# Optimization experiments

Measured on AMD Instinct MI355X. Metric: run time of the kernel, lower is better.

## Reference

```python
import jax, jax.numpy as jnp
import numpy as np

TOP_K = 6
N_GROUP = 8
TOPK_GROUP = 3
ROUTED_SCALING = 16.0
NORM_TOPK_PROB = False


def setup_inputs() -> dict:
    key = jax.random.key(0)
    k1, k2 = jax.random.split(key)
    hidden_states = jax.random.normal(k1, (4, 4096, 5120), dtype=jnp.float32)
    weight = jax.random.normal(k2, (160, 5120), dtype=jnp.float32) * 0.02
    return {"hidden_states": hidden_states, "weight": weight}


def _gate(hidden_states, weight):
    B, S, H = hidden_states.shape
    E = weight.shape[0]
    x = hidden_states.reshape(-1, H).astype(jnp.float32)  # [T, H]
    logits = jnp.einsum('th,eh->te', x, weight.astype(jnp.float32))  # [T, E]
    scores = jax.nn.softmax(logits, axis=-1)
    # group_limited_greedy: restrict experts to the topk_group best groups
    G = N_GROUP
    group_scores = scores.reshape(-1, G, E // G).max(axis=-1)  # [T, G]
    _, group_idx = jax.lax.top_k(group_scores, TOPK_GROUP)  # [T, topk_group]
    group_mask = jax.nn.one_hot(group_idx, G, dtype=jnp.bool_).any(axis=1)  # [T, G]
    score_mask = jnp.repeat(group_mask, E // G, axis=-1)  # [T, E]
    tmp_scores = jnp.where(score_mask, scores, 0.0)
    topk_weight, topk_idx = jax.lax.top_k(tmp_scores, TOP_K)
    if TOP_K > 1 and NORM_TOPK_PROB:
        topk_weight = topk_weight / (topk_weight.sum(axis=-1, keepdims=True) + 1e-20)
    else:
        topk_weight = topk_weight * ROUTED_SCALING
    return topk_idx, topk_weight


def reference(hidden_states, weight):
    return _gate(hidden_states, weight)
```

## Files before the change

kernel.cpp:

```cpp
#include <hip/hip_runtime.h>
#include <math.h>


#define TT    16384
#define HH    5120
#define EE    160
#define BT    32
#define BK    32
#define NT    (HH / BK)
#define SXLD  36
#define SWLD  161
#define SLF   161
#define TOPK  6

__device__ __forceinline__ bool betterf(float va, int ia, float vb, int ib) {
    return (va > vb) || ((va == vb) && (ia < ib));
}

__global__ __launch_bounds__(256)
void gate_kernel(const float* __restrict__ X, const float* __restrict__ W,
                 float* __restrict__ out) {
    __shared__ __align__(16) unsigned char smem_raw[2*BK*SXLD*4 + 2*BK*SWLD*4];
    float* sx    = (float*)smem_raw;
    float* sw    = sx + 2 * BK * SXLD;
    float* slogf = (float*)smem_raw;

    const int tid = threadIdx.x;
    const int tx  = tid & 31;
    const int ty  = tid >> 5;
    const long tok0 = (long)blockIdx.x * BT;

    double acc[4][5];
    #pragma unroll
    for (int j = 0; j < 4; ++j)
        #pragma unroll
        for (int m = 0; m < 5; ++m) acc[j][m] = 0.0;

    float4 px, pw[5];

    {
        int i = tid, tl = i >> 3, k4 = (i & 7) << 2;
        px = *(const float4*)(X + (tok0 + tl) * HH + k4);
        #pragma unroll
        for (int r = 0; r < 5; ++r) {
            int q = tid + 256 * r, e = q >> 3, kk = (q & 7) << 2;
            pw[r] = *(const float4*)(W + (long)e * HH + kk);
        }
        sx[(k4 + 0) * SXLD + tl] = px.x;
        sx[(k4 + 1) * SXLD + tl] = px.y;
        sx[(k4 + 2) * SXLD + tl] = px.z;
        sx[(k4 + 3) * SXLD + tl] = px.w;
        #pragma unroll
        for (int r = 0; r < 5; ++r) {
            int q = tid + 256 * r, e = q >> 3, kk = (q & 7) << 2;
            sw[(kk + 0) * SWLD + e] = pw[r].x;
            sw[(kk + 1) * SWLD + e] = pw[r].y;
            sw[(kk + 2) * SWLD + e] = pw[r].z;
            sw[(kk + 3) * SWLD + e] = pw[r].w;
        }
    }
    __syncthreads();

    for (int t = 0; t < NT; ++t) {
        const int cur = t & 1;
        if (t + 1 < NT) {
            const int k0 = (t + 1) * BK;
            int i = tid, tl = i >> 3, k4 = (i & 7) << 2;
            px = *(const float4*)(X + (tok0 + tl) * HH + k0 + k4);
            #pragma unroll
            for (int r = 0; r < 5; ++r) {
                int q = tid + 256 * r, e = q >> 3, kk = (q & 7) << 2;
                pw[r] = *(const float4*)(W + (long)e * HH + k0 + kk);
            }
        }
        const float* bx = sx + cur * (BK * SXLD);
        const float* bw = sw + cur * (BK * SWLD);
        #pragma unroll 4
        for (int k = 0; k < BK; ++k) {
            float4 xa = *(const float4*)(bx + k * SXLD + 4 * ty);
            double xd[4] = {(double)xa.x, (double)xa.y, (double)xa.z, (double)xa.w};
            double wd[5];
            #pragma unroll
            for (int m = 0; m < 5; ++m) wd[m] = (double)bw[k * SWLD + tx + 32 * m];
            #pragma unroll
            for (int j = 0; j < 4; ++j)
                #pragma unroll
                for (int m = 0; m < 5; ++m)
                    acc[j][m] = fma(xd[j], wd[m], acc[j][m]);
        }
        if (t + 1 < NT) {
            const int nb = (t + 1) & 1;
            float* wxp = sx + nb * (BK * SXLD);
            float* wwp = sw + nb * (BK * SWLD);
            int i = tid, tl = i >> 3, k4 = (i & 7) << 2;
            wxp[(k4 + 0) * SXLD + tl] = px.x;
            wxp[(k4 + 1) * SXLD + tl] = px.y;
            wxp[(k4 + 2) * SXLD + tl] = px.z;
            wxp[(k4 + 3) * SXLD + tl] = px.w;
            #pragma unroll
            for (int r = 0; r < 5; ++r) {
                int q = tid + 256 * r, e = q >> 3, kk = (q & 7) << 2;
                wwp[(kk + 0) * SWLD + e] = pw[r].x;
                wwp[(kk + 1) * SWLD + e] = pw[r].y;
                wwp[(kk + 2) * SWLD + e] = pw[r].z;
                wwp[(kk + 3) * SWLD + e] = pw[r].w;
            }
        }
        __syncthreads();
    }

    #pragma unroll
    for (int j = 0; j < 4; ++j)
        #pragma unroll
        for (int m = 0; m < 5; ++m)
            slogf[(4 * ty + j) * SLF + tx + 32 * m] = (float)acc[j][m];
    __syncthreads();

    const int token = tid >> 3;
    const int sub   = tid & 7;
    const float* rowp = slogf + token * SLF + sub * 20;
    float l[20];
    #pragma unroll
    for (int i = 0; i < 20; ++i) l[i] = rowp[i];

    float gm = l[0];
    #pragma unroll
    for (int i = 1; i < 20; ++i) gm = fmaxf(gm, l[i]);
    float mxf = gm;
    mxf = fmaxf(mxf, __shfl_xor(mxf, 1));
    mxf = fmaxf(mxf, __shfl_xor(mxf, 2));
    mxf = fmaxf(mxf, __shfl_xor(mxf, 4));

    #pragma unroll
    for (int i = 0; i < 20; ++i) l[i] = expf(l[i] - mxf);
    float sef = 0.f;
    #pragma unroll
    for (int i = 0; i < 20; ++i) sef += l[i];
    sef += __shfl_xor(sef, 1);
    sef += __shfl_xor(sef, 2);
    sef += __shfl_xor(sef, 4);
    #pragma unroll
    for (int i = 0; i < 20; ++i) l[i] = l[i] / sef;

    float gs = l[0];
    #pragma unroll
    for (int i = 1; i < 20; ++i) gs = fmaxf(gs, l[i]);

    float a0 = gs;
    float a1 = __shfl_xor(a0, 1);
    float a2 = __shfl_xor(a0, 2), a3 = __shfl_xor(a1, 2);
    float a4 = __shfl_xor(a0, 4), a5 = __shfl_xor(a1, 4);
    float a6 = __shfl_xor(a2, 4), a7 = __shfl_xor(a3, 4);
    float gv[8] = {a0, a1, a2, a3, a4, a5, a6, a7};
    int   gi[8] = {sub, sub^1, sub^2, sub^3, sub^4, sub^5, sub^6, sub^7};

    int tg0, tg1, tg2;
    {
        float bv; int bi;
        bv = gv[0]; bi = gi[0];
        #pragma unroll
        for (int q = 1; q < 8; ++q) if (betterf(gv[q], gi[q], bv, bi)) { bv = gv[q]; bi = gi[q]; }
        tg0 = bi;
        #pragma unroll
        for (int q = 0; q < 8; ++q) if (gi[q] == tg0) gv[q] = -INFINITY;
        bv = gv[0]; bi = gi[0];
        #pragma unroll
        for (int q = 1; q < 8; ++q) if (betterf(gv[q], gi[q], bv, bi)) { bv = gv[q]; bi = gi[q]; }
        tg1 = bi;
        #pragma unroll
        for (int q = 0; q < 8; ++q) if (gi[q] == tg1) gv[q] = -INFINITY;
        bv = gv[0]; bi = gi[0];
        #pragma unroll
        for (int q = 1; q < 8; ++q) if (betterf(gv[q], gi[q], bv, bi)) { bv = gv[q]; bi = gi[q]; }
        tg2 = bi;
    }
    const bool allowed = (sub == tg0) || (sub == tg1) || (sub == tg2);

    float v[6]; int ix[6];
    #pragma unroll
    for (int j = 0; j < 6; ++j) { v[j] = -INFINITY; ix[j] = 1 << 30; }
    #pragma unroll
    for (int i = 0; i < 20; ++i) {
        const float val = allowed ? l[i] : -INFINITY;
        const int   idx = sub * 20 + i;
        if (betterf(val, idx, v[5], ix[5])) {
            v[5] = val; ix[5] = idx;
            #pragma unroll
            for (int j = 5; j >= 1; --j)
                if (betterf(v[j], ix[j], v[j-1], ix[j-1])) {
                    float tv = v[j]; v[j] = v[j-1]; v[j-1] = tv;
                    int   ti = ix[j]; ix[j] = ix[j-1]; ix[j-1] = ti;
                }
        }
    }

    #pragma unroll
    for (int st = 1; st <= 4; st <<= 1) {
        float pv[6]; int pix[6];
        #pragma unroll
        for (int j = 0; j < 6; ++j) {
            pv[j]  = __shfl_xor(v[j], st);
            pix[j] = __shfl_xor(ix[j], st);
        }
        #pragma unroll
        for (int j = 0; j < 6; ++j) {
            const float val = pv[j]; const int idx = pix[j];
            if (betterf(val, idx, v[5], ix[5])) {
                v[5] = val; ix[5] = idx;
                #pragma unroll
                for (int q = 5; q >= 1; --q)
                    if (betterf(v[q], ix[q], v[q-1], ix[q-1])) {
                        float tv = v[q]; v[q] = v[q-1]; v[q-1] = tv;
                        int   ti = ix[q]; ix[q] = ix[q-1]; ix[q-1] = ti;
                    }
            }
        }
    }

    if (sub == 0) {
        const long tokg = tok0 + token;
        #pragma unroll
        for (int j = 0; j < 6; ++j) {
            out[tokg * TOPK + j] = (float)ix[j];
            out[(long)TT * TOPK + tokg * TOPK + j] = 16.0f * v[j];
        }
    }
}

extern "C" void kernel_launch(void* const* d_in, const int* in_sizes, int n_in,
                              void* d_out, int out_size, void* d_ws, size_t ws_size,
                              hipStream_t stream) {
    const float* X = (const float*)d_in[0];
    const float* W = (const float*)d_in[1];
    float* out = (float*)d_out;
    gate_kernel<<<TT / BT, 256, 0, stream>>>(X, W, out);
}
```

Before: 1.040 ms.

## Use fp32 GEMM with fp64 recompute fallback for near-tie tokens

```diff
diff --git a/kernel.cpp b/kernel.cpp
--- a/kernel.cpp
+++ b/kernel.cpp
@@ -12,6 +12,7 @@
 #define SWLD  161
 #define SLF   161
 #define TOPK  6
+#define TH    3e-4f
 
 __device__ __forceinline__ bool betterf(float va, int ia, float vb, int ib) {
     return (va > vb) || ((va == vb) && (ia < ib));
@@ -21,6 +22,7 @@
 void gate_kernel(const float* __restrict__ X, const float* __restrict__ W,
                  float* __restrict__ out) {
     __shared__ __align__(16) unsigned char smem_raw[2*BK*SXLD*4 + 2*BK*SWLD*4];
+    __shared__ int sFlags[BT];
     float* sx    = (float*)smem_raw;
     float* sw    = sx + 2 * BK * SXLD;
     float* slogf = (float*)smem_raw;
@@ -30,11 +32,11 @@
     const int ty  = tid >> 5;
     const long tok0 = (long)blockIdx.x * BT;
 
-    double acc[4][5];
+    float acc[4][5];
     #pragma unroll
     for (int j = 0; j < 4; ++j)
         #pragma unroll
-        for (int m = 0; m < 5; ++m) acc[j][m] = 0.0;
+        for (int m = 0; m < 5; ++m) acc[j][m] = 0.f;
 
     float4 px, pw[5];
 
@@ -78,15 +80,15 @@
         #pragma unroll 4
         for (int k = 0; k < BK; ++k) {
             float4 xa = *(const float4*)(bx + k * SXLD + 4 * ty);
-            double xd[4] = {(double)xa.x, (double)xa.y, (double)xa.z, (double)xa.w};
-            double wd[5];
-            #pragma unroll
-            for (int m = 0; m < 5; ++m) wd[m] = (double)bw[k * SWLD + tx + 32 * m];
+            float wv[5];
+            #pragma unroll
+            for (int m = 0; m < 5; ++m) wv[m] = bw[k * SWLD + tx + 32 * m];
+            float xv[4] = {xa.x, xa.y, xa.z, xa.w};
             #pragma unroll
             for (int j = 0; j < 4; ++j)
                 #pragma unroll
                 for (int m = 0; m < 5; ++m)
-                    acc[j][m] = fma(xd[j], wd[m], acc[j][m]);
+                    acc[j][m] = fmaf(xv[j], wv[m], acc[j][m]);
         }
         if (t + 1 < NT) {
             const int nb = (t + 1) & 1;
@@ -113,116 +115,249 @@
     for (int j = 0; j < 4; ++j)
         #pragma unroll
         for (int m = 0; m < 5; ++m)
-            slogf[(4 * ty + j) * SLF + tx + 32 * m] = (float)acc[j][m];
+            slogf[(4 * ty + j) * SLF + tx + 32 * m] = acc[j][m];
     __syncthreads();
 
     const int token = tid >> 3;
     const int sub   = tid & 7;
-    const float* rowp = slogf + token * SLF + sub * 20;
-    float l[20];
-    #pragma unroll
-    for (int i = 0; i < 20; ++i) l[i] = rowp[i];
-
-    float gm = l[0];
-    #pragma unroll
-    for (int i = 1; i < 20; ++i) gm = fmaxf(gm, l[i]);
-    float mxf = gm;
-    mxf = fmaxf(mxf, __shfl_xor(mxf, 1));
-    mxf = fmaxf(mxf, __shfl_xor(mxf, 2));
-    mxf = fmaxf(mxf, __shfl_xor(mxf, 4));
-
-    #pragma unroll
-    for (int i = 0; i < 20; ++i) l[i] = expf(l[i] - mxf);
-    float sef = 0.f;
-    #pragma unroll
-    for (int i = 0; i < 20; ++i) sef += l[i];
-    sef += __shfl_xor(sef, 1);
-    sef += __shfl_xor(sef, 2);
-    sef += __shfl_xor(sef, 4);
-    #pragma unroll
-    for (int i = 0; i < 20; ++i) l[i] = l[i] / sef;
-
-    float gs = l[0];
-    #pragma unroll
-    for (int i = 1; i < 20; ++i) gs = fmaxf(gs, l[i]);
-
-    float a0 = gs;
-    float a1 = __shfl_xor(a0, 1);
-    float a2 = __shfl_xor(a0, 2), a3 = __shfl_xor(a1, 2);
-    float a4 = __shfl_xor(a0, 4), a5 = __shfl_xor(a1, 4);
-    float a6 = __shfl_xor(a2, 4), a7 = __shfl_xor(a3, 4);
-    float gv[8] = {a0, a1, a2, a3, a4, a5, a6, a7};
-    int   gi[8] = {sub, sub^1, sub^2, sub^3, sub^4, sub^5, sub^6, sub^7};
-
-    int tg0, tg1, tg2;
     {
-        float bv; int bi;
-        bv = gv[0]; bi = gi[0];
-        #pragma unroll
-        for (int q = 1; q < 8; ++q) if (betterf(gv[q], gi[q], bv, bi)) { bv = gv[q]; bi = gi[q]; }
-        tg0 = bi;
-        #pragma unroll
-        for (int q = 0; q < 8; ++q) if (gi[q] == tg0) gv[q] = -INFINITY;
-        bv = gv[0]; bi = gi[0];
-        #pragma unroll
-        for (int q = 1; q < 8; ++q) if (betterf(gv[q], gi[q], bv, bi)) { bv = gv[q]; bi = gi[q]; }
-        tg1 = bi;
-        #pragma unroll
-        for (int q = 0; q < 8; ++q) if (gi[q] == tg1) gv[q] = -INFINITY;
-        bv = gv[0]; bi = gi[0];
-        #pragma unroll
-        for (int q = 1; q < 8; ++q) if (betterf(gv[q], gi[q], bv, bi)) { bv = gv[q]; bi = gi[q]; }
-        tg2 = bi;
-    }
-    const bool allowed = (sub == tg0) || (sub == tg1) || (sub == tg2);
-
-    float v[6]; int ix[6];
-    #pragma unroll
-    for (int j = 0; j < 6; ++j) { v[j] = -INFINITY; ix[j] = 1 << 30; }
-    #pragma unroll
-    for (int i = 0; i < 20; ++i) {
-        const float val = allowed ? l[i] : -INFINITY;
-        const int   idx = sub * 20 + i;
-        if (betterf(val, idx, v[5], ix[5])) {
-            v[5] = val; ix[5] = idx;
-            #pragma unroll
-            for (int j = 5; j >= 1; --j)
-                if (betterf(v[j], ix[j], v[j-1], ix[j-1])) {
-                    float tv = v[j]; v[j] = v[j-1]; v[j-1] = tv;
-                    int   ti = ix[j]; ix[j] = ix[j-1]; ix[j-1] = ti;
+        const float* rowp = slogf + token * SLF + sub * 20;
+        float l[20];
+        #pragma unroll
+        for (int i = 0; i < 20; ++i) l[i] = rowp[i];
+
+        float gm = l[0];
+        #pragma unroll
+        for (int i = 1; i < 20; ++i) gm = fmaxf(gm, l[i]);
+        float mx = gm;
+        mx = fmaxf(mx, __shfl_xor(mx, 1));
+        mx = fmaxf(mx, __shfl_xor(mx, 2));
+        mx = fmaxf(mx, __shfl_xor(mx, 4));
+        float sef = 0.f;
+        #pragma unroll
+        for (int i = 0; i < 20; ++i) sef += expf(l[i] - mx);
+        sef += __shfl_xor(sef, 1);
+        sef += __shfl_xor(sef, 2);
+        sef += __shfl_xor(sef, 4);
+
+        float a0 = gm;
+        float a1 = __shfl_xor(a0, 1);
+        float a2 = __shfl_xor(a0, 2), a3 = __shfl_xor(a1, 2);
+        float a4 = __shfl_xor(a0, 4), a5 = __shfl_xor(a1, 4);
+        float a6 = __shfl_xor(a2, 4), a7 = __shfl_xor(a3, 4);
+        float gv[8] = {a0, a1, a2, a3, a4, a5, a6, a7};
+        int   gi[8] = {sub, sub^1, sub^2, sub^3, sub^4, sub^5, sub^6, sub^7};
+
+        int tg0, tg1, tg2; float g3v, g4v;
+        {
+            float bv; int bi;
+            bv = gv[0]; bi = gi[0];
+            #pragma unroll
+            for (int q = 1; q < 8; ++q) if (betterf(gv[q], gi[q], bv, bi)) { bv = gv[q]; bi = gi[q]; }
+            tg0 = bi;
+            #pragma unroll
+            for (int q = 0; q < 8; ++q) if (gi[q] == tg0) gv[q] = -INFINITY;
+            bv = gv[0]; bi = gi[0];
+            #pragma unroll
+            for (int q = 1; q < 8; ++q) if (betterf(gv[q], gi[q], bv, bi)) { bv = gv[q]; bi = gi[q]; }
+            tg1 = bi;
+            #pragma unroll
+            for (int q = 0; q < 8; ++q) if (gi[q] == tg1) gv[q] = -INFINITY;
+            bv = gv[0]; bi = gi[0];
+            #pragma unroll
+            for (int q = 1; q < 8; ++q) if (betterf(gv[q], gi[q], bv, bi)) { bv = gv[q]; bi = gi[q]; }
+            tg2 = bi; g3v = bv;
+            #pragma unroll
+            for (int q = 0; q < 8; ++q) if (gi[q] == tg2) gv[q] = -INFINITY;
+            bv = gv[0];
+            #pragma unroll
+            for (int q = 1; q < 8; ++q) bv = fmaxf(bv, gv[q]);
+            g4v = bv;
+        }
+        const bool allowed = (sub == tg0) || (sub == tg1) || (sub == tg2);
+
+        float v[7]; int ix[7];
+        #pragma unroll
+        for (int j = 0; j < 7; ++j) { v[j] = -INFINITY; ix[j] = 1 << 30; }
+        #pragma unroll
+        for (int i = 0; i < 20; ++i) {
+            const float val = allowed ? l[i] : -INFINITY;
+            const int   idx = sub * 20 + i;
+            if (betterf(val, idx, v[6], ix[6])) {
+                v[6] = val; ix[6] = idx;
+                #pragma unroll
+                for (int j = 6; j >= 1; --j)
+                    if (betterf(v[j], ix[j], v[j-1], ix[j-1])) {
+                        float tv = v[j]; v[j] = v[j-1]; v[j-1] = tv;
+                        int   ti = ix[j]; ix[j] = ix[j-1]; ix[j-1] = ti;
+                    }
+            }
+        }
+        #pragma unroll
+        for (int st = 1; st <= 4; st <<= 1) {
+            float pv[7]; int pix[7];
+            #pragma unroll
+            for (int j = 0; j < 7; ++j) {
+                pv[j]  = __shfl_xor(v[j], st);
+                pix[j] = __shfl_xor(ix[j], st);
+            }
+            #pragma unroll
+            for (int j = 0; j < 7; ++j) {
+                const float val = pv[j]; const int idx = pix[j];
+                if (betterf(val, idx, v[6], ix[6])) {
+                    v[6] = val; ix[6] = idx;
+                    #pragma unroll
+                    for (int q = 6; q >= 1; --q)
+                        if (betterf(v[q], ix[q], v[q-1], ix[q-1])) {
+                            float tv = v[q]; v[q] = v[q-1]; v[q-1] = tv;
+                            int   ti = ix[q]; ix[q] = ix[q-1]; ix[q-1] = ti;
+                        }
                 }
-        }
-    }
-
-    #pragma unroll
-    for (int st = 1; st <= 4; st <<= 1) {
-        float pv[6]; int pix[6];
-        #pragma unroll
-        for (int j = 0; j < 6; ++j) {
-            pv[j]  = __shfl_xor(v[j], st);
-            pix[j] = __shfl_xor(ix[j], st);
-        }
-        #pragma unroll
-        for (int j = 0; j < 6; ++j) {
-            const float val = pv[j]; const int idx = pix[j];
+            }
+        }
+
+        float mingap = g3v - g4v;
+        #pragma unroll
+        for (int j = 0; j < 6; ++j) mingap = fminf(mingap, v[j] - v[j+1]);
+        const int flag = (mingap < TH) ? 1 : 0;
+
+        if (sub == 0) {
+            sFlags[token] = flag;
+            const long tokg = tok0 + token;
+            #pragma unroll
+            for (int j = 0; j < 6; ++j) {
+                out[tokg * TOPK + j] = (float)ix[j];
+                out[(long)TT * TOPK + tokg * TOPK + j] =
+                    16.0f * expf(v[j] - mx) / sef;
+            }
+        }
+    }
+    __syncthreads();
+
+    for (int ft = 0; ft < BT; ++ft) {
+        if (sFlags[ft] && tid < EE) {
+            const float* xr = X + (tok0 + ft) * HH;
+            const float* wr = W + (long)tid * HH;
+            double c0 = 0.0, c1 = 0.0, c2 = 0.0, c3 = 0.0;
+            for (int k = 0; k < HH; k += 4) {
+                float4 xv = *(const float4*)(xr + k);
+                float4 wv = *(const float4*)(wr + k);
+                c0 = fma((double)xv.x, (double)wv.x, c0);
+                c1 = fma((double)xv.y, (double)wv.y, c1);
+                c2 = fma((double)xv.z, (double)wv.z, c2);
+                c3 = fma((double)xv.w, (double)wv.w, c3);
+            }
+            slogf[ft * SLF + tid] = (float)((c0 + c1) + (c2 + c3));
+        }
+    }
+    __syncthreads();
+
+    if (sFlags[token]) {
+        const float* rowp = slogf + token * SLF + sub * 20;
+        float l[20];
+        #pragma unroll
+        for (int i = 0; i < 20; ++i) l[i] = rowp[i];
+
+        float gm = l[0];
+        #pragma unroll
+        for (int i = 1; i < 20; ++i) gm = fmaxf(gm, l[i]);
+        float mxf = gm;
+        mxf = fmaxf(mxf, __shfl_xor(mxf, 1));
+        mxf = fmaxf(mxf, __shfl_xor(mxf, 2));
+        mxf = fmaxf(mxf, __shfl_xor(mxf, 4));
+
+        #pragma unroll
+        for (int i = 0; i < 20; ++i) l[i] = expf(l[i] - mxf);
+        float sef = 0.f;
+        #pragma unroll
+        for (int i = 0; i < 20; ++i) sef += l[i];
+        sef += __shfl_xor(sef, 1);
+        sef += __shfl_xor(sef, 2);
+        sef += __shfl_xor(sef, 4);
+        #pragma unroll
+        for (int i = 0; i < 20; ++i) l[i] = l[i] / sef;
+
+        float gs = l[0];
+        #pragma unroll
+        for (int i = 1; i < 20; ++i) gs = fmaxf(gs, l[i]);
+
+        float a0 = gs;
+        float a1 = __shfl_xor(a0, 1);
+        float a2 = __shfl_xor(a0, 2), a3 = __shfl_xor(a1, 2);
+        float a4 = __shfl_xor(a0, 4), a5 = __shfl_xor(a1, 4);
+        float a6 = __shfl_xor(a2, 4), a7 = __shfl_xor(a3, 4);
+        float gv[8] = {a0, a1, a2, a3, a4, a5, a6, a7};
+        int   gi[8] = {sub, sub^1, sub^2, sub^3, sub^4, sub^5, sub^6, sub^7};
+
+        int tg0, tg1, tg2;
+        {
+            float bv; int bi;
+            bv = gv[0]; bi = gi[0];
+            #pragma unroll
+            for (int q = 1; q < 8; ++q) if (betterf(gv[q], gi[q], bv, bi)) { bv = gv[q]; bi = gi[q]; }
+            tg0 = bi;
+            #pragma unroll
+            for (int q = 0; q < 8; ++q) if (gi[q] == tg0) gv[q] = -INFINITY;
+            bv = gv[0]; bi = gi[0];
+            #pragma unroll
+            for (int q = 1; q < 8; ++q) if (betterf(gv[q], gi[q], bv, bi)) { bv = gv[q]; bi = gi[q]; }
+            tg1 = bi;
+            #pragma unroll
+            for (int q = 0; q < 8; ++q) if (gi[q] == tg1) gv[q] = -INFINITY;
+            bv = gv[0]; bi = gi[0];
+            #pragma unroll
+            for (int q = 1; q < 8; ++q) if (betterf(gv[q], gi[q], bv, bi)) { bv = gv[q]; bi = gi[q]; }
+            tg2 = bi;
+        }
+        const bool allowed = (sub == tg0) || (sub == tg1) || (sub == tg2);
+
+        float v[6]; int ix[6];
+        #pragma unroll
+        for (int j = 0; j < 6; ++j) { v[j] = -INFINITY; ix[j] = 1 << 30; }
+        #pragma unroll
+        for (int i = 0; i < 20; ++i) {
+            const float val = allowed ? l[i] : -INFINITY;
+            const int   idx = sub * 20 + i;
             if (betterf(val, idx, v[5], ix[5])) {
                 v[5] = val; ix[5] = idx;
                 #pragma unroll
-                for (int q = 5; q >= 1; --q)
-                    if (betterf(v[q], ix[q], v[q-1], ix[q-1])) {
-                        float tv = v[q]; v[q] = v[q-1]; v[q-1] = tv;
-                        int   ti = ix[q]; ix[q] = ix[q-1]; ix[q-1] = ti;
+                for (int j = 5; j >= 1; --j)
+                    if (betterf(v[j], ix[j], v[j-1], ix[j-1])) {
+                        float tv = v[j]; v[j] = v[j-1]; v[j-1] = tv;
+                        int   ti = ix[j]; ix[j] = ix[j-1]; ix[j-1] = ti;
                     }
             }
         }
-    }
-
-    if (sub == 0) {
-        const long tokg = tok0 + token;
-        #pragma unroll
-        for (int j = 0; j < 6; ++j) {
-            out[tokg * TOPK + j] = (float)ix[j];
-            out[(long)TT * TOPK + tokg * TOPK + j] = 16.0f * v[j];
+        #pragma unroll
+        for (int st = 1; st <= 4; st <<= 1) {
+            float pv[6]; int pix[6];
+            #pragma unroll
+            for (int j = 0; j < 6; ++j) {
+                pv[j]  = __shfl_xor(v[j], st);
+                pix[j] = __shfl_xor(ix[j], st);
+            }
+            #pragma unroll
+            for (int j = 0; j < 6; ++j) {
+                const float val = pv[j]; const int idx = pix[j];
+                if (betterf(val, idx, v[5], ix[5])) {
+                    v[5] = val; ix[5] = idx;
+                    #pragma unroll
+                    for (int q = 5; q >= 1; --q)
+                        if (betterf(v[q], ix[q], v[q-1], ix[q-1])) {
+                            float tv = v[q]; v[q] = v[q-1]; v[q-1] = tv;
+                            int   ti = ix[q]; ix[q] = ix[q-1]; ix[q-1] = ti;
+                        }
+                }
+            }
+        }
+
+        if (sub == 0) {
+            const long tokg = tok0 + token;
+            #pragma unroll
+            for (int j = 0; j < 6; ++j) {
+                out[tokg * TOPK + j] = (float)ix[j];
+                out[(long)TT * TOPK + tokg * TOPK + j] = 16.0f * v[j];
+            }
         }
     }
 }
```

Result: slower. 1.166 ms (+12.0%).
